# Optimization experiments

Hardware: AMD Instinct MI355X
Metric: run time of the kernel (lower is better)

## Reference

```python
import jax, jax.numpy as jnp
import numpy as np
from jax import lax

B, D, C = 4096, 128, 101  # batch, input_dim (evidence sources), num_class+1 (incl. omega)


def setup_inputs() -> dict:
    key = jax.random.key(0)
    # non-negative mass assignments (uniform [0,1)) so the normalizing sum is positive
    inputs = jax.random.uniform(key, (B, D, C), dtype=jnp.float32)
    return {"inputs": inputs}


def reference(inputs) -> jnp.ndarray:
    """Sequential Dempster-Shafer combination across the input_dim axis.

    inputs: (B, D, C) where the last channel C-1 is the omega (ignorance) mass.
    Returns the fused, normalized mass (B, C).
    """
    m_init = inputs[:, 0, :]                      # (B, C)
    rest = jnp.moveaxis(inputs[:, 1:, :], 1, 0)   # (D-1, B, C) scan over sources

    def step(m1, m2):
        omega1 = m1[:, -1:]                       # (B, 1)
        omega2 = m2[:, -1:]                       # (B, 1)
        c = m1 * m2 + m1 * omega2 + omega1 * m2   # unnormalized combined mass
        c = c / jnp.sum(c, axis=-1, keepdims=True)
        return c, None

    m_final, _ = lax.scan(step, m_init, rest)
    return m_final
```

## Files before the change

### kernel.cpp

```cpp
#include <hip/hip_runtime.h>
#include <stdint.h>


constexpr int kB   = 4096;
constexpr int kD   = 128;
constexpr int kC   = 101;
constexpr int kRow = kD * kC;

__global__ __launch_bounds__(256, 4) void ds_scan_kernel(const float* __restrict__ in,
                                                         float* __restrict__ out) {
    const int tid  = threadIdx.x;
    const int rloc = tid >> 7;
    const int j    = tid & 127;
    const int b    = blockIdx.x * 2 + rloc;
    const bool live = j < kC;
    const int  jc   = live ? j : (kC - 1);

    const float* __restrict__ base = in + (size_t)b * kRow;

    const float nu0 = base[kC - 1];
    float M = base[jc] + nu0;
    float w = nu0;
    int   E = 0;

    auto step = [&](int t) {
        const float* __restrict__ r = base + t * kC;
        const float xt = r[jc];
        const float nt = r[kC - 1];
        const float Xi = xt + nt;
        const float P  = w * nt;
        const float P2 = P + P;
        M = fmaf(M, Xi, P2);
        w = P + P2;
    };
    auto renorm = [&]() {
        const float s = M + w;
        const uint32_t eb = (__float_as_uint(s) >> 23) & 0xFFu;
        const float scale = __uint_as_float((254u - eb) << 23);
        M *= scale; w *= scale;
        E += (int)eb - 127;
    };

    int t = 1;
    #pragma unroll
    for (int s = 0; s < 7; ++s, ++t) step(t);
    for (int g = 0; g < 15; ++g) {
        #pragma unroll
        for (int s = 0; s < 8; ++s, ++t) step(t);
        renorm();
    }

    float v  = live ? (M - w) : 0.0f;
    int   Ee = live ? E : (int)0xC0000000;

    int em = Ee;
    #pragma unroll
    for (int off = 32; off >= 1; off >>= 1) em = max(em, __shfl_xor(em, off));

    __shared__ int   sE[4];
    __shared__ float sV[4];
    const int wave = tid >> 6;
    if ((tid & 63) == 0) sE[wave] = em;
    __syncthreads();
    const int w0   = rloc * 2;
    const int Emax = max(sE[w0], sE[w0 + 1]);

    const int d = (live ? E : 0) - Emax;
    const float sc = (d < -126) ? 0.0f
                   : __uint_as_float((uint32_t)(d + 127) << 23);
    v *= sc;

    float sv = v;
    #pragma unroll
    for (int off = 32; off >= 1; off >>= 1) sv += __shfl_xor(sv, off);
    if ((tid & 63) == 0) sV[wave] = sv;
    __syncthreads();
    const float S = sV[w0] + sV[w0 + 1];

    if (live) out[(size_t)b * kC + j] = v / S;
}

extern "C" void kernel_launch(void* const* d_in, const int* in_sizes, int n_in,
                              void* d_out, int out_size, void* d_ws, size_t ws_size,
                              hipStream_t stream) {
    const float* in = (const float*)d_in[0];
    float* out = (float*)d_out;
    ds_scan_kernel<<<kB / 2, 256, 0, stream>>>(in, out);
}
```

Before: 36.19 us.

## Map one wavefront per batch row with paired-class vector loads

Each 64-lane wavefront now handles one batch row instead of two rows per 128-thread group. Each lane owns two adjacent classes, fetched with a single 8-byte load. The omega mass is broadcast with a lane shuffle from lane 50 instead of a separate scalar load per step. Because a row fits in one wavefront, the final max-exponent and sum reductions need no shared memory or block barriers. The tradeoffs are 8-byte accesses that are only 4-byte aligned, since rows have an odd float stride, and a cross-lane shuffle inside the serial recurrence.

```diff
diff --git a/kernel.cpp b/kernel.cpp
--- a/kernel.cpp
+++ b/kernel.cpp
@@ -7,37 +7,43 @@
 constexpr int kC   = 101;
 constexpr int kRow = kD * kC;
 
-__global__ __launch_bounds__(256, 4) void ds_scan_kernel(const float* __restrict__ in,
-                                                         float* __restrict__ out) {
-    const int tid  = threadIdx.x;
-    const int rloc = tid >> 7;
-    const int j    = tid & 127;
-    const int b    = blockIdx.x * 2 + rloc;
-    const bool live = j < kC;
-    const int  jc   = live ? j : (kC - 1);
+typedef float f2 __attribute__((ext_vector_type(2)));
 
+__device__ __forceinline__ f2 load_f2(const float* p) {
+    f2 v; __builtin_memcpy(&v, p, 8); return v;
+}
+
+__global__ __launch_bounds__(256, 4) void ds_scan2_kernel(const float* __restrict__ in,
+                                                          float* __restrict__ out) {
+    const int lane = threadIdx.x & 63;
+    const int wave = threadIdx.x >> 6;
+    const int b    = blockIdx.x * 4 + wave;
+
+    const bool pair_live = lane < 50;
+    const int  off       = pair_live ? 2 * lane : 99;
     const float* __restrict__ base = in + (size_t)b * kRow;
 
-    const float nu0 = base[kC - 1];
-    float M = base[jc] + nu0;
-    float w = nu0;
-    int   E = 0;
+    f2 v = load_f2(base + off);
+    const float nu0 = __shfl(v.y, 50);
+    float M0 = v.x + nu0;
+    float M1 = v.y + nu0;
+    float w  = nu0;
+    int   E  = 0;
 
     auto step = [&](int t) {
-        const float* __restrict__ r = base + t * kC;
-        const float xt = r[jc];
-        const float nt = r[kC - 1];
-        const float Xi = xt + nt;
-        const float P  = w * nt;
+        const f2 x = load_f2(base + t * kC + off);
+        const float n  = __shfl(x.y, 50);
+        const float P  = w * n;
         const float P2 = P + P;
-        M = fmaf(M, Xi, P2);
-        w = P + P2;
+        M0 = fmaf(M0, x.x + n, P2);
+        M1 = fmaf(M1, x.y + n, P2);
+        w  = P + P2;
     };
     auto renorm = [&]() {
-        const float s = M + w;
+        const float s = M0 + M1 + w;
         const uint32_t eb = (__float_as_uint(s) >> 23) & 0xFFu;
         const float scale = __uint_as_float((254u - eb) << 23);
-        M *= scale; w *= scale;
+        M0 *= scale; M1 *= scale; w *= scale;
         E += (int)eb - 127;
     };
 
@@ -50,34 +56,29 @@
         renorm();
     }
 
-    float v  = live ? (M - w) : 0.0f;
-    int   Ee = live ? E : (int)0xC0000000;
+    int em = E;
+    #pragma unroll
+    for (int o = 32; o >= 1; o >>= 1) em = max(em, __shfl_xor(em, o));
 
-    int em = Ee;
-    #pragma unroll
-    for (int off = 32; off >= 1; off >>= 1) em = max(em, __shfl_xor(em, off));
-
-    __shared__ int   sE[4];
-    __shared__ float sV[4];
-    const int wave = tid >> 6;
-    if ((tid & 63) == 0) sE[wave] = em;
-    __syncthreads();
-    const int w0   = rloc * 2;
-    const int Emax = max(sE[w0], sE[w0 + 1]);
-
-    const int d = (live ? E : 0) - Emax;
+    const int d = E - em;
     const float sc = (d < -126) ? 0.0f
                    : __uint_as_float((uint32_t)(d + 127) << 23);
-    v *= sc;
 
-    float sv = v;
+    float v0 = pair_live   ? (M0 - w) * sc : 0.0f;
+    float v1 = (lane <= 50) ? (M1 - w) * sc : 0.0f;
+
+    float sv = v0 + v1;
     #pragma unroll
-    for (int off = 32; off >= 1; off >>= 1) sv += __shfl_xor(sv, off);
-    if ((tid & 63) == 0) sV[wave] = sv;
-    __syncthreads();
-    const float S = sV[w0] + sV[w0 + 1];
+    for (int o = 32; o >= 1; o >>= 1) sv += __shfl_xor(sv, o);
+    const float S = sv;
 
-    if (live) out[(size_t)b * kC + j] = v / S;
+    float* __restrict__ o = out + (size_t)b * kC;
+    if (pair_live) {
+        f2 r; r.x = v0 / S; r.y = v1 / S;
+        __builtin_memcpy(o + off, &r, 8);
+    } else if (lane == 50) {
+        o[100] = v1 / S;
+    }
 }
 
 extern "C" void kernel_launch(void* const* d_in, const int* in_sizes, int n_in,
@@ -85,5 +86,5 @@
                               hipStream_t stream) {
     const float* in = (const float*)d_in[0];
     float* out = (float*)d_out;
-    ds_scan_kernel<<<kB / 2, 256, 0, stream>>>(in, out);
+    ds_scan2_kernel<<<kB / 4, 256, 0, stream>>>(in, out);
 }
```

Measured after the change: 35.80 us. About the same (-1.1%).
